# Kernel optimization log

Hardware: AMD Instinct MI355X
Metric: run time of the kernel (lower is better)

Reference implementation:

```python
import jax, jax.numpy as jnp
import numpy as np

N_QUBITS = 6
N_LAYERS = 8
N_CLASSES = 4
BATCH = 262144
DIM = 2 ** N_QUBITS  # 64


def setup_inputs() -> dict:
    key = jax.random.key(0)
    k1, k2, k3, k4 = jax.random.split(key, 4)
    x = jax.random.normal(k1, (BATCH, DIM), dtype=jnp.float32)
    # TorchLayer default init for StronglyEntanglingLayers weights: U(0, 2*pi)
    weights = jax.random.uniform(k2, (N_LAYERS, N_QUBITS, 3), dtype=jnp.float32,
                                 minval=0.0, maxval=2.0 * np.pi)
    fc_w = jax.random.normal(k3, (N_CLASSES, N_QUBITS), dtype=jnp.float32) * 0.3
    fc_b = jax.random.normal(k4, (N_CLASSES,), dtype=jnp.float32) * 0.1
    return {"x": x, "weights": weights, "fc_w": fc_w, "fc_b": fc_b}


def _rot_mats(weights):
    # PennyLane Rot(phi, theta, omega) = RZ(omega) RY(theta) RZ(phi)
    phi, theta, omega = weights[..., 0], weights[..., 1], weights[..., 2]
    c = jnp.cos(theta / 2)
    s = jnp.sin(theta / 2)
    m00 = jnp.exp(-0.5j * (phi + omega)) * c
    m01 = -jnp.exp(0.5j * (phi - omega)) * s
    m10 = jnp.exp(-0.5j * (phi - omega)) * s
    m11 = jnp.exp(0.5j * (phi + omega)) * c
    # [L, n, 2, 2] complex64
    return jnp.stack([jnp.stack([m00, m01], -1), jnp.stack([m10, m11], -1)], -2).astype(jnp.complex64)


def _apply_1q(state, U, q):
    # state: [B, 2, 2, 2, 2, 2, 2]; apply 2x2 gate U on qubit axis q+1
    ax = q + 1
    s = jnp.moveaxis(state, ax, -1)
    s = jnp.einsum('ij,...j->...i', U, s)
    return jnp.moveaxis(s, -1, ax)


def _cnot(state, c, t):
    # flip target qubit t on the control==1 slice of qubit c
    axc = c + 1
    s0 = jax.lax.index_in_dim(state, 0, axis=axc, keepdims=False)
    s1 = jax.lax.index_in_dim(state, 1, axis=axc, keepdims=False)
    t_ax = t + 1 if t < c else t  # target axis after removing control axis
    s1 = jnp.flip(s1, axis=t_ax)
    return jnp.stack([s0, s1], axis=axc)


def _pauli_z_signs():
    # qubit 0 is the most significant bit of the basis-state index
    bits = (jnp.arange(DIM)[:, None] >> jnp.arange(N_QUBITS - 1, -1, -1)[None, :]) & 1
    return (1 - 2 * bits).astype(jnp.float32)  # [DIM, N_QUBITS]


def reference(x, weights, fc_w, fc_b):
    B = x.shape[0]
    # F.normalize(p=2) + AmplitudeEmbedding(normalize=True) -> single L2 normalize
    xn = x / jnp.maximum(jnp.linalg.norm(x, axis=1, keepdims=True), 1e-12)
    state = xn.astype(jnp.complex64).reshape((B,) + (2,) * N_QUBITS)
    U = _rot_mats(weights)  # [L, n, 2, 2]
    for l in range(N_LAYERS):
        for q in range(N_QUBITS):
            state = _apply_1q(state, U[l, q], q)
        r = (l % (N_QUBITS - 1)) + 1  # StronglyEntanglingLayers default ranges
        for q in range(N_QUBITS):
            state = _cnot(state, q, (q + r) % N_QUBITS)
    probs = (state.real ** 2 + state.imag ** 2).reshape(B, DIM)
    expvals = probs @ _pauli_z_signs()  # [B, n] <Z_i>
    return expvals @ fc_w.T + fc_b
```

## Files before the change

### kernel.cpp

```cpp
#include <hip/hip_runtime.h>

#define NQ 6
#define DIM 64
#define NL 8

#define KP  136
#define ROWS 128

typedef __attribute__((ext_vector_type(8))) short short8v;
typedef __attribute__((ext_vector_type(4))) float floatx4;

__device__ inline short f2bf_rne(float f) {
    unsigned u = __float_as_uint(f);
    u += 0x7FFF + ((u >> 16) & 1);
    return (short)(u >> 16);
}

__global__ __launch_bounds__(64) void qnn_prep(
    const float* __restrict__ wts,
    const float* __restrict__ fc_w,
    void* __restrict__ ws)
{
    __shared__ float gc[48][4];
    const int n   = threadIdx.x;
    const int col = blockIdx.x;

    if (n < 48) {
        float phi = wts[n*3+0], th = wts[n*3+1], om = wts[n*3+2];
        float ch = cosf(0.5f*th), sh = sinf(0.5f*th);
        float p  = 0.5f*(phi+om), m  = 0.5f*(phi-om);
        gc[n][0] = cosf(p)*ch;
        gc[n][1] = sinf(p)*ch;
        gc[n][2] = cosf(m)*sh;
        gc[n][3] = sinf(m)*sh;
    }
    __syncthreads();

    float ar = (n == col) ? 1.0f : 0.0f;
    float ai = 0.0f;

    #pragma unroll
    for (int l = 0; l < NL; ++l) {
        #pragma unroll
        for (int q = 0; q < NQ; ++q) {
            const int g     = l*NQ + q;
            const int shift = 5 - q;
            const int mask  = 1 << shift;
            const int b     = (n >> shift) & 1;
            const float cpch = gc[g][0];
            const float spch = gc[g][1];
            const float cmsh = gc[g][2];
            const float smsh = gc[g][3];
            const float pr = __shfl_xor(ar, mask, 64);
            const float pi = __shfl_xor(ai, mask, 64);
            const float udr = cpch;
            const float udi = b ?  spch : -spch;
            const float uor = b ?  cmsh : -cmsh;
            const float uoi = -smsh;
            const float nr = udr*ar - udi*ai + uor*pr - uoi*pi;
            const float ni = udr*ai + udi*ar + uor*pi + uoi*pr;
            ar = nr; ai = ni;
        }
        const int r = (l % (NQ - 1)) + 1;
        #pragma unroll
        for (int q = 0; q < NQ; ++q) {
            const int t     = (q + r) % NQ;
            const int cmask = 1 << (5 - q);
            const int tmask = 1 << (5 - t);
            const float pr = __shfl_xor(ar, tmask, 64);
            const float pi = __shfl_xor(ai, tmask, 64);
            const bool ctrl = (n & cmask) != 0;
            ar = ctrl ? pr : ar;
            ai = ctrl ? pi : ai;
        }
    }

    unsigned short* Bs = (unsigned short*)ws;
    unsigned short hr = (unsigned short)f2bf_rne(ar);
    float hrf = __uint_as_float((unsigned)hr << 16);
    unsigned short lr = (unsigned short)f2bf_rne(ar - hrf);
    unsigned short hi = (unsigned short)f2bf_rne(ai);
    float hif = __uint_as_float((unsigned)hi << 16);
    unsigned short li = (unsigned short)f2bf_rne(ai - hif);
    Bs[n*KP + col]           = hr;
    Bs[n*KP + 64 + col]      = lr;
    Bs[(64+n)*KP + col]      = hi;
    Bs[(64+n)*KP + 64 + col] = li;

    if (col == 0) {
        float m0=0.f, m1=0.f, m2=0.f, m3=0.f;
        #pragma unroll
        for (int q = 0; q < NQ; ++q) {
            const float sgn = 1.0f - 2.0f*(float)((n >> (5-q)) & 1);
            m0 = fmaf(sgn, fc_w[0*NQ+q], m0);
            m1 = fmaf(sgn, fc_w[1*NQ+q], m1);
            m2 = fmaf(sgn, fc_w[2*NQ+q], m2);
            m3 = fmaf(sgn, fc_w[3*NQ+q], m3);
        }
        float* Mo = (float*)((char*)ws + 128*KP*2);
        Mo[n*4+0]=m0; Mo[n*4+1]=m1; Mo[n*4+2]=m2; Mo[n*4+3]=m3;
    }
}

__global__ __launch_bounds__(256, 2) void qnn_main(
    const float* __restrict__ x,
    const float* __restrict__ fc_b,
    const void* __restrict__ wsv,
    float* __restrict__ out)
{
    __shared__ __align__(16) unsigned short Bs[128*KP];
    __shared__ float Ml[DIM*4];

    const int tid = threadIdx.x;
    const int s0  = blockIdx.x * ROWS;
    const int lane = tid & 63;
    const int w    = tid >> 6;
    const int l15  = lane & 15;
    const int quad = lane >> 4;

    {
        const floatx4* bg = (const floatx4*)wsv;
        floatx4* bl = (floatx4*)Bs;
        #pragma unroll
        for (int i = 0; i < 9; ++i) {
            int idx = tid + i*256;
            if (idx < 128*KP*2/16) bl[idx] = bg[idx];
        }
        const float* Mg = (const float*)((const char*)wsv + 128*KP*2);
        Ml[tid] = Mg[tid];
    }

    short8v afr[2][2];
    #pragma unroll
    for (int mt = 0; mt < 2; ++mt) {
        const size_t row = (size_t)(s0 + w*32 + mt*16 + l15);
        const float* xp = x + row*DIM + quad*8;
        #pragma unroll
        for (int h = 0; h < 2; ++h) {
            float4 u0 = *(const float4*)(xp + h*32);
            float4 u1 = *(const float4*)(xp + h*32 + 4);
            short8v a;
            a[0]=f2bf_rne(u0.x); a[1]=f2bf_rne(u0.y);
            a[2]=f2bf_rne(u0.z); a[3]=f2bf_rne(u0.w);
            a[4]=f2bf_rne(u1.x); a[5]=f2bf_rne(u1.y);
            a[6]=f2bf_rne(u1.z); a[7]=f2bf_rne(u1.w);
            afr[mt][h] = a;
        }
    }
    __syncthreads();

    floatx4 acc[2][8];
    #pragma unroll
    for (int mt = 0; mt < 2; ++mt)
        #pragma unroll
        for (int nt = 0; nt < 8; ++nt)
            acc[mt][nt] = (floatx4){0.f, 0.f, 0.f, 0.f};

    #pragma unroll
    for (int kk = 0; kk < 4; ++kk) {
        const int h  = kk & 1;
        const int bk = (kk << 5) + quad*8;
        #pragma unroll
        for (int nt = 0; nt < 8; ++nt) {
            short8v b = *(const short8v*)&Bs[(nt*16 + l15)*KP + bk];
            acc[0][nt] = __builtin_amdgcn_mfma_f32_16x16x32_bf16(afr[0][h], b, acc[0][nt], 0, 0, 0);
            acc[1][nt] = __builtin_amdgcn_mfma_f32_16x16x32_bf16(afr[1][h], b, acc[1][nt], 0, 0, 0);
        }
    }

    floatx4 Mv[4];
    #pragma unroll
    for (int nt = 0; nt < 4; ++nt)
        Mv[nt] = *(const floatx4*)&Ml[(nt*16 + l15)*4];

    float q[2][4][5];
    #pragma unroll
    for (int mt = 0; mt < 2; ++mt)
        #pragma unroll
        for (int r = 0; r < 4; ++r)
            #pragma unroll
            for (int c = 0; c < 5; ++c) q[mt][r][c] = 0.f;

    #pragma unroll
    for (int mt = 0; mt < 2; ++mt)
        #pragma unroll
        for (int nt = 0; nt < 4; ++nt)
            #pragma unroll
            for (int r = 0; r < 4; ++r) {
                const float re = acc[mt][nt][r];
                const float im = acc[mt][nt + 4][r];
                const float p  = fmaf(re, re, im*im);
                q[mt][r][0] = fmaf(p, Mv[nt][0], q[mt][r][0]);
                q[mt][r][1] = fmaf(p, Mv[nt][1], q[mt][r][1]);
                q[mt][r][2] = fmaf(p, Mv[nt][2], q[mt][r][2]);
                q[mt][r][3] = fmaf(p, Mv[nt][3], q[mt][r][3]);
                q[mt][r][4] += p;
            }

    #pragma unroll
    for (int mt = 0; mt < 2; ++mt)
        #pragma unroll
        for (int r = 0; r < 4; ++r)
            #pragma unroll
            for (int c = 0; c < 5; ++c) {
                float v = q[mt][r][c];
                v += __shfl_xor(v, 1, 64);
                v += __shfl_xor(v, 2, 64);
                v += __shfl_xor(v, 4, 64);
                v += __shfl_xor(v, 8, 64);
                q[mt][r][c] = v;
            }

    const float b0 = fc_b[0], b1 = fc_b[1], b2 = fc_b[2], b3 = fc_b[3];
    #pragma unroll
    for (int mt = 0; mt < 2; ++mt)
        #pragma unroll
        for (int r = 0; r < 4; ++r) {
            const float inv = 1.0f / q[mt][r][4];
            float4 o;
            o.x = fmaf(q[mt][r][0], inv, b0);
            o.y = fmaf(q[mt][r][1], inv, b1);
            o.z = fmaf(q[mt][r][2], inv, b2);
            o.w = fmaf(q[mt][r][3], inv, b3);
            if (l15 == mt*4 + r) {
                const int srow = w*32 + mt*16 + quad*4 + r;
                *(float4*)(out + (size_t)(s0 + srow)*4) = o;
            }
        }
}

extern "C" void kernel_launch(void* const* d_in, const int* in_sizes, int n_in,
                              void* d_out, int out_size, void* d_ws, size_t ws_size,
                              hipStream_t stream) {
    const float* x    = (const float*)d_in[0];
    const float* wts  = (const float*)d_in[1];
    const float* fc_w = (const float*)d_in[2];
    const float* fc_b = (const float*)d_in[3];
    float* out = (float*)d_out;

    const int batch = in_sizes[0] / DIM;

    qnn_prep<<<DIM, DIM, 0, stream>>>(wts, fc_w, d_ws);
    qnn_main<<<batch / ROWS, 256, 0, stream>>>(x, fc_b, d_ws, out);
}
```

Baseline: 116.3 us.

## Compute class readout with fp16 MFMA instead of per-lane FMAs and shuffles

```diff
diff --git a/kernel.cpp b/kernel.cpp
--- a/kernel.cpp
+++ b/kernel.cpp
@@ -7,8 +7,9 @@
 #define KP  136
 #define ROWS 128
 
-typedef __attribute__((ext_vector_type(8))) short short8v;
-typedef __attribute__((ext_vector_type(4))) float floatx4;
+typedef __attribute__((ext_vector_type(8))) short    short8v;
+typedef __attribute__((ext_vector_type(4))) float    floatx4;
+typedef __attribute__((ext_vector_type(4))) _Float16 half4v;
 
 __device__ inline short f2bf_rne(float f) {
     unsigned u = __float_as_uint(f);
@@ -88,17 +89,29 @@
     Bs[(64+n)*KP + 64 + col] = li;
 
     if (col == 0) {
-        float m0=0.f, m1=0.f, m2=0.f, m3=0.f;
-        #pragma unroll
-        for (int q = 0; q < NQ; ++q) {
-            const float sgn = 1.0f - 2.0f*(float)((n >> (5-q)) & 1);
-            m0 = fmaf(sgn, fc_w[0*NQ+q], m0);
-            m1 = fmaf(sgn, fc_w[1*NQ+q], m1);
-            m2 = fmaf(sgn, fc_w[2*NQ+q], m2);
-            m3 = fmaf(sgn, fc_w[3*NQ+q], m3);
-        }
-        float* Mo = (float*)((char*)ws + 128*KP*2);
-        Mo[n*4+0]=m0; Mo[n*4+1]=m1; Mo[n*4+2]=m2; Mo[n*4+3]=m3;
+        const int cp = n & 15;
+        const int qd = n >> 4;
+        half4v* Mo = (half4v*)((char*)ws + 128*KP*2);
+        #pragma unroll
+        for (int c2 = 0; c2 < 4; ++c2) {
+            half4v h4;
+            #pragma unroll
+            for (int j = 0; j < 4; ++j) {
+                const int i = c2*16 + qd*4 + j;
+                float v = 0.f;
+                if (cp < 4) {
+                    #pragma unroll
+                    for (int q = 0; q < NQ; ++q) {
+                        const float sgn = 1.0f - 2.0f*(float)((i >> (5-q)) & 1);
+                        v = fmaf(sgn, fc_w[cp*NQ + q], v);
+                    }
+                } else if (cp == 4) {
+                    v = 1.0f;
+                }
+                h4[j] = (_Float16)v;
+            }
+            Mo[c2*64 + n] = h4;
+        }
     }
 }
 
@@ -109,10 +122,9 @@
     float* __restrict__ out)
 {
     __shared__ __align__(16) unsigned short Bs[128*KP];
-    __shared__ float Ml[DIM*4];
-
-    const int tid = threadIdx.x;
-    const int s0  = blockIdx.x * ROWS;
+
+    const int tid  = threadIdx.x;
+    const int s0   = blockIdx.x * ROWS;
     const int lane = tid & 63;
     const int w    = tid >> 6;
     const int l15  = lane & 15;
@@ -126,14 +138,12 @@
             int idx = tid + i*256;
             if (idx < 128*KP*2/16) bl[idx] = bg[idx];
         }
-        const float* Mg = (const float*)((const char*)wsv + 128*KP*2);
-        Ml[tid] = Mg[tid];
-    }
-
-    short8v afr[2][2];
-    #pragma unroll
-    for (int mt = 0; mt < 2; ++mt) {
-        const size_t row = (size_t)(s0 + w*32 + mt*16 + l15);
+    }
+
+    short8v xf[2][2];
+    #pragma unroll
+    for (int st = 0; st < 2; ++st) {
+        const size_t row = (size_t)(s0 + w*32 + st*16 + l15);
         const float* xp = x + row*DIM + quad*8;
         #pragma unroll
         for (int h = 0; h < 2; ++h) {
@@ -144,89 +154,65 @@
             a[2]=f2bf_rne(u0.z); a[3]=f2bf_rne(u0.w);
             a[4]=f2bf_rne(u1.x); a[5]=f2bf_rne(u1.y);
             a[6]=f2bf_rne(u1.z); a[7]=f2bf_rne(u1.w);
-            afr[mt][h] = a;
+            xf[st][h] = a;
         }
     }
     __syncthreads();
 
     floatx4 acc[2][8];
     #pragma unroll
-    for (int mt = 0; mt < 2; ++mt)
-        #pragma unroll
-        for (int nt = 0; nt < 8; ++nt)
-            acc[mt][nt] = (floatx4){0.f, 0.f, 0.f, 0.f};
+    for (int st = 0; st < 2; ++st)
+        #pragma unroll
+        for (int mt = 0; mt < 8; ++mt)
+            acc[st][mt] = (floatx4){0.f, 0.f, 0.f, 0.f};
 
     #pragma unroll
     for (int kk = 0; kk < 4; ++kk) {
         const int h  = kk & 1;
         const int bk = (kk << 5) + quad*8;
-        #pragma unroll
-        for (int nt = 0; nt < 8; ++nt) {
-            short8v b = *(const short8v*)&Bs[(nt*16 + l15)*KP + bk];
-            acc[0][nt] = __builtin_amdgcn_mfma_f32_16x16x32_bf16(afr[0][h], b, acc[0][nt], 0, 0, 0);
-            acc[1][nt] = __builtin_amdgcn_mfma_f32_16x16x32_bf16(afr[1][h], b, acc[1][nt], 0, 0, 0);
-        }
-    }
-
-    floatx4 Mv[4];
-    #pragma unroll
-    for (int nt = 0; nt < 4; ++nt)
-        Mv[nt] = *(const floatx4*)&Ml[(nt*16 + l15)*4];
-
-    float q[2][4][5];
-    #pragma unroll
-    for (int mt = 0; mt < 2; ++mt)
-        #pragma unroll
-        for (int r = 0; r < 4; ++r)
-            #pragma unroll
-            for (int c = 0; c < 5; ++c) q[mt][r][c] = 0.f;
-
-    #pragma unroll
-    for (int mt = 0; mt < 2; ++mt)
-        #pragma unroll
-        for (int nt = 0; nt < 4; ++nt)
+        short8v wf[8];
+        #pragma unroll
+        for (int mt = 0; mt < 8; ++mt)
+            wf[mt] = *(const short8v*)&Bs[(mt*16 + l15)*KP + bk];
+        #pragma unroll
+        for (int mt = 0; mt < 8; ++mt) {
+            acc[0][mt] = __builtin_amdgcn_mfma_f32_16x16x32_bf16(wf[mt], xf[0][h], acc[0][mt], 0, 0, 0);
+            acc[1][mt] = __builtin_amdgcn_mfma_f32_16x16x32_bf16(wf[mt], xf[1][h], acc[1][mt], 0, 0, 0);
+        }
+    }
+
+    const half4v* Mg = (const half4v*)((const char*)wsv + 128*KP*2);
+    half4v a2[4];
+    #pragma unroll
+    for (int c2 = 0; c2 < 4; ++c2) a2[c2] = Mg[c2*64 + lane];
+
+    const float b0 = fc_b[0], b1 = fc_b[1], b2 = fc_b[2], b3 = fc_b[3];
+
+    #pragma unroll
+    for (int st = 0; st < 2; ++st) {
+        floatx4 d2 = (floatx4){0.f, 0.f, 0.f, 0.f};
+        #pragma unroll
+        for (int c2 = 0; c2 < 4; ++c2) {
+            half4v pb;
             #pragma unroll
             for (int r = 0; r < 4; ++r) {
-                const float re = acc[mt][nt][r];
-                const float im = acc[mt][nt + 4][r];
-                const float p  = fmaf(re, re, im*im);
-                q[mt][r][0] = fmaf(p, Mv[nt][0], q[mt][r][0]);
-                q[mt][r][1] = fmaf(p, Mv[nt][1], q[mt][r][1]);
-                q[mt][r][2] = fmaf(p, Mv[nt][2], q[mt][r][2]);
-                q[mt][r][3] = fmaf(p, Mv[nt][3], q[mt][r][3]);
-                q[mt][r][4] += p;
+                const float re = acc[st][c2][r];
+                const float im = acc[st][c2 + 4][r];
+                pb[r] = (_Float16)fmaf(re, re, im*im);
             }
-
-    #pragma unroll
-    for (int mt = 0; mt < 2; ++mt)
-        #pragma unroll
-        for (int r = 0; r < 4; ++r)
-            #pragma unroll
-            for (int c = 0; c < 5; ++c) {
-                float v = q[mt][r][c];
-                v += __shfl_xor(v, 1, 64);
-                v += __shfl_xor(v, 2, 64);
-                v += __shfl_xor(v, 4, 64);
-                v += __shfl_xor(v, 8, 64);
-                q[mt][r][c] = v;
-            }
-
-    const float b0 = fc_b[0], b1 = fc_b[1], b2 = fc_b[2], b3 = fc_b[3];
-    #pragma unroll
-    for (int mt = 0; mt < 2; ++mt)
-        #pragma unroll
-        for (int r = 0; r < 4; ++r) {
-            const float inv = 1.0f / q[mt][r][4];
+            d2 = __builtin_amdgcn_mfma_f32_16x16x16f16(a2[c2], pb, d2, 0, 0, 0);
+        }
+        const float ssv = __shfl_xor(d2[0], 16, 64);
+        if (quad == 0) {
+            const float inv = 1.0f / ssv;
             float4 o;
-            o.x = fmaf(q[mt][r][0], inv, b0);
-            o.y = fmaf(q[mt][r][1], inv, b1);
-            o.z = fmaf(q[mt][r][2], inv, b2);
-            o.w = fmaf(q[mt][r][3], inv, b3);
-            if (l15 == mt*4 + r) {
-                const int srow = w*32 + mt*16 + quad*4 + r;
-                *(float4*)(out + (size_t)(s0 + srow)*4) = o;
-            }
-        }
+            o.x = fmaf(d2[0], inv, b0);
+            o.y = fmaf(d2[1], inv, b1);
+            o.z = fmaf(d2[2], inv, b2);
+            o.w = fmaf(d2[3], inv, b3);
+            *(float4*)(out + (size_t)(s0 + w*32 + st*16 + l15)*4) = o;
+        }
+    }
 }
 
 extern "C" void kernel_launch(void* const* d_in, const int* in_sizes, int n_in,
```

After: 109.3 us. 6.0% less time.
